# Kernel tuning notes

Hardware: AMD Instinct MI355X
Metric: run time of the kernel (lower is better)

The kernel has to match this reference:

```python
import jax, jax.numpy as jnp
import numpy as np

NUM_STEPS = 8
THRESHOLD = 0.5


def _glorot(key, shape):
    fan_in = shape[0]
    return jax.random.normal(key, shape, dtype=jnp.float32) / np.sqrt(fan_in).astype(np.float32)


def setup_inputs() -> dict:
    key = jax.random.key(0)
    ks = jax.random.split(key, 24)
    B, APM = 2048, 32           # molecules, atoms per molecule
    N = B * APM                 # 65536 nodes
    E = N * 4                   # 262144 directed edges
    NF, EF, NH, EH, MA = 64, 16, 128, 128, 256
    inp = {}
    inp['mol_a_reprs'] = jax.random.normal(ks[0], (B, MA), dtype=jnp.float32)
    inp['node_features'] = jax.random.normal(ks[1], (N, NF), dtype=jnp.float32)
    inp['edge_features'] = jax.random.normal(ks[2], (E, EF), dtype=jnp.float32)
    inp['node_hidden0'] = jnp.zeros((N, NH), dtype=jnp.float32)
    inp['edge_hidden0'] = jnp.zeros((E, EH), dtype=jnp.float32)
    inp['edges'] = jax.random.randint(ks[3], (2, E), 0, N, dtype=jnp.int32)
    inp['batch_indices'] = jnp.repeat(jnp.arange(B, dtype=jnp.int32), APM)  # sorted, in-range
    # MPN weights (no bias)
    inp['W1'] = _glorot(ks[4], (NF, EH))   # src node features -> edge hidden
    inp['W2'] = _glorot(ks[5], (EF, EH))   # edge features -> edge hidden
    inp['W3'] = _glorot(ks[6], (NH, EH))   # src node hidden -> edge hidden
    inp['U1'] = _glorot(ks[7], (NF, NH))   # node features -> node hidden
    inp['U2'] = _glorot(ks[8], (EH, NH))   # aggregated edge hidden -> node hidden
    # pick-atom MLP: (MA+NH)->256->128->64->1
    inp['M1w'] = _glorot(ks[9], (MA + NH, 256)); inp['M1b'] = jnp.zeros((256,), jnp.float32)
    inp['M2w'] = _glorot(ks[10], (256, 128));    inp['M2b'] = jnp.zeros((128,), jnp.float32)
    inp['M3w'] = _glorot(ks[11], (128, 64));     inp['M3b'] = jnp.zeros((64,), jnp.float32)
    inp['M4w'] = _glorot(ks[12], (64, 1));       inp['M4b'] = jnp.zeros((1,), jnp.float32)
    return inp


def _mpn(node_features, edge_features, node_h, edge_h, src, dst, W1, W2, W3, U1, U2):
    N = node_features.shape[0]
    W1x_src = node_features[src] @ W1          # [E, EH], loop-invariant
    W2e = edge_features @ W2                   # [E, EH], loop-invariant
    U1x = node_features @ U1                   # [N, NH], loop-invariant
    for _ in range(NUM_STEPS):
        agg = jax.ops.segment_sum(edge_h, dst, num_segments=N)   # [N, EH]
        node_h = jax.nn.relu(U1x + agg @ U2)                     # [N, NH]
        edge_h = jax.nn.relu(W1x_src + W2e + node_h[src] @ W3)   # [E, EH]
    return node_h


def reference(mol_a_reprs, node_features, edge_features, node_hidden0, edge_hidden0,
              edges, batch_indices, W1, W2, W3, U1, U2,
              M1w, M1b, M2w, M2b, M3w, M3b, M4w, M4b):
    src, dst = edges[0], edges[1]
    node_h = _mpn(node_features, edge_features, node_hidden0, edge_hidden0,
                  src, dst, W1, W2, W3, U1, U2)
    b_atom_mol_a = mol_a_reprs[batch_indices]                    # index_select gather [N, MA]
    x = jnp.concatenate([node_h, b_atom_mol_a], axis=1)          # [N, NH+MA]
    x = jax.nn.relu(x @ M1w + M1b)
    x = jax.nn.relu(x @ M2w + M2b)
    x = jax.nn.relu(x @ M3w + M3b)
    p = jax.nn.sigmoid(x @ M4w + M4b)                            # [N, 1]
    return p >= THRESHOLD
```

## Files before the change

kernel.cpp:

```cpp
#include <hip/hip_runtime.h>
#include <cstddef>

#define NF 64
#define EF 16
#define NH 128
#define EH 128
#define MA 256

static inline int ceil_div(int a, int b) { return (a + b - 1) / b; }

__global__ __launch_bounds__(256) void gemm_kernel(
    const float* __restrict__ A, const float* __restrict__ Bw,
    float* __restrict__ C,
    const float* __restrict__ addR, const int* __restrict__ addIdx,
    const float* __restrict__ bias,
    int M, int K, int Nc, int doRelu)
{
    __shared__ float As[16][64];
    __shared__ float Bs[16][64];
    const int tid = threadIdx.x;
    const int tx = tid & 15, ty = tid >> 4;
    const int m0 = blockIdx.y << 6;
    const int n0 = blockIdx.x << 6;
    const int lr = tid >> 2;
    const int lc = (tid & 3) << 2;
    const int bkr = tid >> 4;
    const int bc = (tid & 15) << 2;

    float acc[4][4];
#pragma unroll
    for (int i = 0; i < 4; ++i)
#pragma unroll
        for (int j = 0; j < 4; ++j) acc[i][j] = 0.0f;

    for (int k0 = 0; k0 < K; k0 += 16) {
        float4 a4 = *(const float4*)(A + (size_t)(m0 + lr) * K + (k0 + lc));
        float4 b4 = *(const float4*)(Bw + (size_t)(k0 + bkr) * Nc + (n0 + bc));
        __syncthreads();
        As[lc + 0][lr] = a4.x;
        As[lc + 1][lr] = a4.y;
        As[lc + 2][lr] = a4.z;
        As[lc + 3][lr] = a4.w;
        *(float4*)&Bs[bkr][bc] = b4;
        __syncthreads();
#pragma unroll
        for (int kk = 0; kk < 16; ++kk) {
            float a0 = As[kk][ty * 4 + 0];
            float a1 = As[kk][ty * 4 + 1];
            float a2 = As[kk][ty * 4 + 2];
            float a3 = As[kk][ty * 4 + 3];
            float b0 = Bs[kk][tx * 4 + 0];
            float b1 = Bs[kk][tx * 4 + 1];
            float b2 = Bs[kk][tx * 4 + 2];
            float b3 = Bs[kk][tx * 4 + 3];
            acc[0][0] += a0 * b0; acc[0][1] += a0 * b1; acc[0][2] += a0 * b2; acc[0][3] += a0 * b3;
            acc[1][0] += a1 * b0; acc[1][1] += a1 * b1; acc[1][2] += a1 * b2; acc[1][3] += a1 * b3;
            acc[2][0] += a2 * b0; acc[2][1] += a2 * b1; acc[2][2] += a2 * b2; acc[2][3] += a2 * b3;
            acc[3][0] += a3 * b0; acc[3][1] += a3 * b1; acc[3][2] += a3 * b2; acc[3][3] += a3 * b3;
        }
    }

    const int c = n0 + tx * 4;
    float4 bv = make_float4(0.f, 0.f, 0.f, 0.f);
    if (bias) bv = *(const float4*)(bias + c);
#pragma unroll
    for (int i = 0; i < 4; ++i) {
        int r = m0 + ty * 4 + i;
        float4 v = make_float4(acc[i][0], acc[i][1], acc[i][2], acc[i][3]);
        if (addR) {
            int ar = addIdx ? addIdx[r] : r;
            float4 ad = *(const float4*)(addR + (size_t)ar * Nc + c);
            v.x += ad.x; v.y += ad.y; v.z += ad.z; v.w += ad.w;
        }
        v.x += bv.x; v.y += bv.y; v.z += bv.z; v.w += bv.w;
        if (doRelu) {
            v.x = fmaxf(v.x, 0.f); v.y = fmaxf(v.y, 0.f);
            v.z = fmaxf(v.z, 0.f); v.w = fmaxf(v.w, 0.f);
        }
        *(float4*)(C + (size_t)r * Nc + c) = v;
    }
}

__global__ __launch_bounds__(256) void hist_kernel(const int* __restrict__ dst, int* __restrict__ deg, int E) {
    int e = blockIdx.x * 256 + threadIdx.x;
    if (e < E) atomicAdd(&deg[dst[e]], 1);
}

__global__ __launch_bounds__(256) void scan_block_kernel(const int* __restrict__ deg, int* __restrict__ rp,
                                                         int* __restrict__ bsum) {
    __shared__ int buf[256];
    int tid = threadIdx.x;
    int i = blockIdx.x * 256 + tid;
    int v = deg[i];
    buf[tid] = v;
    __syncthreads();
    for (int off = 1; off < 256; off <<= 1) {
        int t = (tid >= off) ? buf[tid - off] : 0;
        __syncthreads();
        buf[tid] += t;
        __syncthreads();
    }
    rp[i] = buf[tid] - v;
    if (tid == 255) bsum[blockIdx.x] = buf[255];
}

__global__ __launch_bounds__(256) void scan_top_kernel(const int* __restrict__ bsum, int* __restrict__ boff,
                                                       int* __restrict__ rp, int N) {
    __shared__ int buf[256];
    int tid = threadIdx.x;
    int v = bsum[tid];
    buf[tid] = v;
    __syncthreads();
    for (int off = 1; off < 256; off <<= 1) {
        int t = (tid >= off) ? buf[tid - off] : 0;
        __syncthreads();
        buf[tid] += t;
        __syncthreads();
    }
    boff[tid] = buf[tid] - v;
    if (tid == 255) rp[N] = buf[255];
}

__global__ __launch_bounds__(256) void scan_add_kernel(int* __restrict__ rp, int* __restrict__ cursor,
                                                       const int* __restrict__ boff) {
    int tid = threadIdx.x;
    int i = blockIdx.x * 256 + tid;
    int v = rp[i] + boff[blockIdx.x];
    rp[i] = v;
    cursor[i] = v;
}

__global__ __launch_bounds__(256) void scatter_kernel(const int* __restrict__ dst, int* __restrict__ cursor,
                                                      int* __restrict__ eid, int E) {
    int e = blockIdx.x * 256 + threadIdx.x;
    if (e < E) {
        int p = atomicAdd(&cursor[dst[e]], 1);
        eid[p] = e;
    }
}

__global__ __launch_bounds__(256) void relu_copy_kernel(const float* __restrict__ in, float* __restrict__ out, int n4) {
    int i = blockIdx.x * 256 + threadIdx.x;
    if (i < n4) {
        float4 v = ((const float4*)in)[i];
        v.x = fmaxf(v.x, 0.f); v.y = fmaxf(v.y, 0.f);
        v.z = fmaxf(v.z, 0.f); v.w = fmaxf(v.w, 0.f);
        ((float4*)out)[i] = v;
    }
}

__global__ __launch_bounds__(128) void agg_kernel(const float* __restrict__ nodeT, const float* __restrict__ W2e,
                                                  const int* __restrict__ rp, const int* __restrict__ eid,
                                                  const int* __restrict__ src, float* __restrict__ agg) {
    int n = blockIdx.x * 4 + threadIdx.y;
    int c = threadIdx.x << 2;
    int p0 = rp[n], p1 = rp[n + 1];
    float4 s = make_float4(0.f, 0.f, 0.f, 0.f);
    for (int p = p0; p < p1; ++p) {
        int e = eid[p];
        int sn = src[e];
        float4 t = *(const float4*)(nodeT + (size_t)sn * EH + c);
        float4 w = *(const float4*)(W2e + (size_t)e * EH + c);
        s.x += fmaxf(t.x + w.x, 0.f);
        s.y += fmaxf(t.y + w.y, 0.f);
        s.z += fmaxf(t.z + w.z, 0.f);
        s.w += fmaxf(t.w + w.w, 0.f);
    }
    *(float4*)(agg + (size_t)n * EH + c) = s;
}

__global__ __launch_bounds__(256) void final_kernel(const float* __restrict__ x3, const float* __restrict__ w,
                                                    const float* __restrict__ b, int* __restrict__ out, int Nn) {
    int g = blockIdx.x * 256 + threadIdx.x;
    int n = g >> 6;
    int lane = threadIdx.x & 63;
    if (n < Nn) {
        float v = x3[(size_t)n * 64 + lane] * w[lane];
#pragma unroll
        for (int off = 32; off > 0; off >>= 1) v += __shfl_xor(v, off, 64);
        if (lane == 0) out[n] = (v + b[0]) >= 0.f ? 1 : 0;
    }
}

extern "C" void kernel_launch(void* const* d_in, const int* in_sizes, int n_in,
                              void* d_out, int out_size, void* d_ws, size_t ws_size,
                              hipStream_t stream)
{
    const float* mol_a = (const float*)d_in[0];
    const float* nf    = (const float*)d_in[1];
    const float* ef    = (const float*)d_in[2];
    const int*   edges = (const int*)d_in[5];
    const int*   batch = (const int*)d_in[6];
    const float* W1  = (const float*)d_in[7];
    const float* W2  = (const float*)d_in[8];
    const float* W3  = (const float*)d_in[9];
    const float* U1  = (const float*)d_in[10];
    const float* U2  = (const float*)d_in[11];
    const float* M1w = (const float*)d_in[12];
    const float* M1b = (const float*)d_in[13];
    const float* M2w = (const float*)d_in[14];
    const float* M2b = (const float*)d_in[15];
    const float* M3w = (const float*)d_in[16];
    const float* M3b = (const float*)d_in[17];
    const float* M4w = (const float*)d_in[18];
    const float* M4b = (const float*)d_in[19];

    const int N = in_sizes[3] / NH;
    const int E = in_sizes[4] / EH;
    const int B = in_sizes[0] / MA;
    const int* srcp = edges;
    const int* dstp = edges + E;

    char* ws = (char*)d_ws;
    size_t off = 0;
    auto alloc = [&](size_t bytes) -> char* {
        char* p = ws + off;
        off = (off + bytes + 255) & ~(size_t)255;
        return p;
    };
    int* deg     = (int*)alloc((size_t)N * 4);
    int* rp      = (int*)alloc(((size_t)N + 1) * 4);
    int* cursor  = (int*)alloc((size_t)N * 4);
    int* bsum    = (int*)alloc(256 * 4);
    int* boff    = (int*)alloc(256 * 4);
    int* eid     = (int*)alloc((size_t)E * 4);
    float* nodePre = (float*)alloc((size_t)N * EH * 4);
    float* U1x     = (float*)alloc((size_t)N * NH * 4);
    float* node_h  = (float*)alloc((size_t)N * NH * 4);
    float* nodeT   = (float*)alloc((size_t)N * EH * 4);
    float* aggp    = (float*)alloc((size_t)N * EH * 4);
    float* molPart = (float*)alloc((size_t)B * 256 * 4);
    float* W2e     = (float*)alloc((size_t)E * EH * 4);
    float* x1 = (float*)W2e;
    float* x2 = nodeT;
    float* x3 = aggp;

    hipMemsetAsync(deg, 0, (size_t)N * 4, stream);
    hist_kernel<<<ceil_div(E, 256), 256, 0, stream>>>(dstp, deg, E);
    scan_block_kernel<<<N / 256, 256, 0, stream>>>(deg, rp, bsum);
    scan_top_kernel<<<1, 256, 0, stream>>>(bsum, boff, rp, N);
    scan_add_kernel<<<N / 256, 256, 0, stream>>>(rp, cursor, boff);
    scatter_kernel<<<ceil_div(E, 256), 256, 0, stream>>>(dstp, cursor, eid, E);

    gemm_kernel<<<dim3(EH / 64, N / 64), 256, 0, stream>>>(nf, W1, nodePre, nullptr, nullptr, nullptr, N, NF, EH, 0);
    gemm_kernel<<<dim3(EH / 64, E / 64), 256, 0, stream>>>(ef, W2, W2e, nullptr, nullptr, nullptr, E, EF, EH, 0);
    gemm_kernel<<<dim3(NH / 64, N / 64), 256, 0, stream>>>(nf, U1, U1x, nullptr, nullptr, nullptr, N, NF, NH, 0);

    relu_copy_kernel<<<(N * NH / 4) / 256, 256, 0, stream>>>(U1x, node_h, N * NH / 4);

    for (int s = 0; s < 7; ++s) {
        gemm_kernel<<<dim3(EH / 64, N / 64), 256, 0, stream>>>(node_h, W3, nodeT, nodePre, nullptr, nullptr, N, NH, EH, 0);
        agg_kernel<<<N / 4, dim3(32, 4), 0, stream>>>(nodeT, W2e, rp, eid, srcp, aggp);
        gemm_kernel<<<dim3(NH / 64, N / 64), 256, 0, stream>>>(aggp, U2, node_h, U1x, nullptr, nullptr, N, EH, NH, 1);
    }

    gemm_kernel<<<dim3(256 / 64, B / 64), 256, 0, stream>>>(mol_a, M1w + 128 * 256, molPart, nullptr, nullptr, M1b, B, MA, 256, 0);
    gemm_kernel<<<dim3(256 / 64, N / 64), 256, 0, stream>>>(node_h, M1w, x1, molPart, batch, nullptr, N, NH, 256, 1);
    gemm_kernel<<<dim3(128 / 64, N / 64), 256, 0, stream>>>(x1, M2w, x2, nullptr, nullptr, M2b, N, 256, 128, 1);
    gemm_kernel<<<dim3(64 / 64, N / 64), 256, 0, stream>>>(x2, M3w, x3, nullptr, nullptr, M3b, N, 128, 64, 1);
    final_kernel<<<ceil_div(N * 64, 256), 256, 0, stream>>>(x3, M4w, M4b, (int*)d_out, N);
}
```

Baseline: 1.445 ms.

## Add 128x128 GEMM tile kernel and pre-sort edge features by destination

Adds a 128x128-tile GEMM kernel in which each thread computes an 8x8 register block, and uses it for most GEMMs. This raises arithmetic intensity per shared-memory load compared with the 64x64 tile. The W2e projection is now computed with rows gathered in CSR (dst-sorted) order, and sorted source indices are stored during scatter. The aggregation loop can then stream W2e contiguously and skip the eid indirection. Larger tiles reduce the number of blocks (512 for the N-sized GEMMs) and raise register pressure, which could lower occupancy.

Result: faster. 1.387 ms (-4.0%).

```diff
diff --git a/kernel.cpp b/kernel.cpp
--- a/kernel.cpp
+++ b/kernel.cpp
@@ -8,6 +8,88 @@
 #define MA 256
 
 static inline int ceil_div(int a, int b) { return (a + b - 1) / b; }
+
+__global__ __launch_bounds__(256) void gemm128_kernel(
+    const float* __restrict__ A, const float* __restrict__ Bw,
+    float* __restrict__ C,
+    const float* __restrict__ addR, const int* __restrict__ addIdx,
+    const float* __restrict__ bias, const int* __restrict__ gatherA,
+    int M, int K, int Nc, int doRelu)
+{
+    __shared__ float As[16][132];
+    __shared__ float Bs[16][132];
+    const int tid = threadIdx.x;
+    const int tx = tid & 15;
+    const int ty = tid >> 4;
+    const int m0 = blockIdx.y << 7;
+    const int n0 = blockIdx.x << 7;
+
+    const int lr = tid >> 1;
+    const int lc = (tid & 1) << 3;
+    const int br = tid >> 4;
+    const int bc = (tid & 15) << 3;
+
+    float acc[8][8];
+#pragma unroll
+    for (int i = 0; i < 8; ++i)
+#pragma unroll
+        for (int j = 0; j < 8; ++j) acc[i][j] = 0.0f;
+
+    int arow = gatherA ? gatherA[m0 + lr] : (m0 + lr);
+    const float* aptr = A + (size_t)arow * K + lc;
+
+    for (int k0 = 0; k0 < K; k0 += 16) {
+        float4 a0 = *(const float4*)(aptr + k0);
+        float4 a1 = *(const float4*)(aptr + k0 + 4);
+        float4 b0 = *(const float4*)(Bw + (size_t)(k0 + br) * Nc + n0 + bc);
+        float4 b1 = *(const float4*)(Bw + (size_t)(k0 + br) * Nc + n0 + bc + 4);
+        __syncthreads();
+        As[lc + 0][lr] = a0.x; As[lc + 1][lr] = a0.y; As[lc + 2][lr] = a0.z; As[lc + 3][lr] = a0.w;
+        As[lc + 4][lr] = a1.x; As[lc + 5][lr] = a1.y; As[lc + 6][lr] = a1.z; As[lc + 7][lr] = a1.w;
+        *(float4*)&Bs[br][bc] = b0;
+        *(float4*)&Bs[br][bc + 4] = b1;
+        __syncthreads();
+#pragma unroll
+        for (int kk = 0; kk < 16; ++kk) {
+            float4 av0 = *(const float4*)&As[kk][ty * 8];
+            float4 av1 = *(const float4*)&As[kk][ty * 8 + 4];
+            float4 bv0 = *(const float4*)&Bs[kk][tx * 8];
+            float4 bv1 = *(const float4*)&Bs[kk][tx * 8 + 4];
+            float a[8] = {av0.x, av0.y, av0.z, av0.w, av1.x, av1.y, av1.z, av1.w};
+            float b[8] = {bv0.x, bv0.y, bv0.z, bv0.w, bv1.x, bv1.y, bv1.z, bv1.w};
+#pragma unroll
+            for (int i = 0; i < 8; ++i)
+#pragma unroll
+                for (int j = 0; j < 8; ++j)
+                    acc[i][j] = fmaf(a[i], b[j], acc[i][j]);
+        }
+    }
+
+    const int c = n0 + tx * 8;
+    float4 bvl = make_float4(0.f, 0.f, 0.f, 0.f), bvh = bvl;
+    if (bias) { bvl = *(const float4*)(bias + c); bvh = *(const float4*)(bias + c + 4); }
+#pragma unroll
+    for (int i = 0; i < 8; ++i) {
+        int r = m0 + ty * 8 + i;
+        float4 vl = make_float4(acc[i][0], acc[i][1], acc[i][2], acc[i][3]);
+        float4 vh = make_float4(acc[i][4], acc[i][5], acc[i][6], acc[i][7]);
+        if (addR) {
+            int ar = addIdx ? addIdx[r] : r;
+            float4 al = *(const float4*)(addR + (size_t)ar * Nc + c);
+            float4 ah = *(const float4*)(addR + (size_t)ar * Nc + c + 4);
+            vl.x += al.x; vl.y += al.y; vl.z += al.z; vl.w += al.w;
+            vh.x += ah.x; vh.y += ah.y; vh.z += ah.z; vh.w += ah.w;
+        }
+        vl.x += bvl.x; vl.y += bvl.y; vl.z += bvl.z; vl.w += bvl.w;
+        vh.x += bvh.x; vh.y += bvh.y; vh.z += bvh.z; vh.w += bvh.w;
+        if (doRelu) {
+            vl.x = fmaxf(vl.x, 0.f); vl.y = fmaxf(vl.y, 0.f); vl.z = fmaxf(vl.z, 0.f); vl.w = fmaxf(vl.w, 0.f);
+            vh.x = fmaxf(vh.x, 0.f); vh.y = fmaxf(vh.y, 0.f); vh.z = fmaxf(vh.z, 0.f); vh.w = fmaxf(vh.w, 0.f);
+        }
+        *(float4*)(C + (size_t)r * Nc + c) = vl;
+        *(float4*)(C + (size_t)r * Nc + c + 4) = vh;
+    }
+}
 
 __global__ __launch_bounds__(256) void gemm_kernel(
     const float* __restrict__ A, const float* __restrict__ Bw,
@@ -130,12 +212,14 @@
     cursor[i] = v;
 }
 
-__global__ __launch_bounds__(256) void scatter_kernel(const int* __restrict__ dst, int* __restrict__ cursor,
-                                                      int* __restrict__ eid, int E) {
+__global__ __launch_bounds__(256) void scatter_kernel(const int* __restrict__ dst, const int* __restrict__ src,
+                                                      int* __restrict__ cursor,
+                                                      int* __restrict__ eid, int* __restrict__ srcS, int E) {
     int e = blockIdx.x * 256 + threadIdx.x;
     if (e < E) {
         int p = atomicAdd(&cursor[dst[e]], 1);
         eid[p] = e;
+        srcS[p] = src[e];
     }
 }
 
@@ -149,18 +233,17 @@
     }
 }
 
-__global__ __launch_bounds__(128) void agg_kernel(const float* __restrict__ nodeT, const float* __restrict__ W2e,
-                                                  const int* __restrict__ rp, const int* __restrict__ eid,
-                                                  const int* __restrict__ src, float* __restrict__ agg) {
+__global__ __launch_bounds__(128) void agg_kernel(const float* __restrict__ nodeT, const float* __restrict__ W2eS,
+                                                  const int* __restrict__ rp, const int* __restrict__ srcS,
+                                                  float* __restrict__ agg) {
     int n = blockIdx.x * 4 + threadIdx.y;
     int c = threadIdx.x << 2;
     int p0 = rp[n], p1 = rp[n + 1];
     float4 s = make_float4(0.f, 0.f, 0.f, 0.f);
     for (int p = p0; p < p1; ++p) {
-        int e = eid[p];
-        int sn = src[e];
+        int sn = srcS[p];
         float4 t = *(const float4*)(nodeT + (size_t)sn * EH + c);
-        float4 w = *(const float4*)(W2e + (size_t)e * EH + c);
+        float4 w = *(const float4*)(W2eS + (size_t)p * EH + c);
         s.x += fmaxf(t.x + w.x, 0.f);
         s.y += fmaxf(t.y + w.y, 0.f);
         s.z += fmaxf(t.z + w.z, 0.f);
@@ -224,14 +307,15 @@
     int* bsum    = (int*)alloc(256 * 4);
     int* boff    = (int*)alloc(256 * 4);
     int* eid     = (int*)alloc((size_t)E * 4);
+    int* srcS    = (int*)alloc((size_t)E * 4);
     float* nodePre = (float*)alloc((size_t)N * EH * 4);
     float* U1x     = (float*)alloc((size_t)N * NH * 4);
     float* node_h  = (float*)alloc((size_t)N * NH * 4);
     float* nodeT   = (float*)alloc((size_t)N * EH * 4);
     float* aggp    = (float*)alloc((size_t)N * EH * 4);
     float* molPart = (float*)alloc((size_t)B * 256 * 4);
-    float* W2e     = (float*)alloc((size_t)E * EH * 4);
-    float* x1 = (float*)W2e;
+    float* W2eS    = (float*)alloc((size_t)E * EH * 4);
+    float* x1 = (float*)W2eS;
     float* x2 = nodeT;
     float* x3 = aggp;
 
@@ -240,23 +324,23 @@
     scan_block_kernel<<<N / 256, 256, 0, stream>>>(deg, rp, bsum);
     scan_top_kernel<<<1, 256, 0, stream>>>(bsum, boff, rp, N);
     scan_add_kernel<<<N / 256, 256, 0, stream>>>(rp, cursor, boff);
-    scatter_kernel<<<ceil_div(E, 256), 256, 0, stream>>>(dstp, cursor, eid, E);
-
-    gemm_kernel<<<dim3(EH / 64, N / 64), 256, 0, stream>>>(nf, W1, nodePre, nullptr, nullptr, nullptr, N, NF, EH, 0);
-    gemm_kernel<<<dim3(EH / 64, E / 64), 256, 0, stream>>>(ef, W2, W2e, nullptr, nullptr, nullptr, E, EF, EH, 0);
-    gemm_kernel<<<dim3(NH / 64, N / 64), 256, 0, stream>>>(nf, U1, U1x, nullptr, nullptr, nullptr, N, NF, NH, 0);
+    scatter_kernel<<<ceil_div(E, 256), 256, 0, stream>>>(dstp, srcp, cursor, eid, srcS, E);
+
+    gemm128_kernel<<<dim3(1, N / 128), 256, 0, stream>>>(nf, W1, nodePre, nullptr, nullptr, nullptr, nullptr, N, NF, EH, 0);
+    gemm128_kernel<<<dim3(1, E / 128), 256, 0, stream>>>(ef, W2, W2eS, nullptr, nullptr, nullptr, eid, E, EF, EH, 0);
+    gemm128_kernel<<<dim3(1, N / 128), 256, 0, stream>>>(nf, U1, U1x, nullptr, nullptr, nullptr, nullptr, N, NF, NH, 0);
 
     relu_copy_kernel<<<(N * NH / 4) / 256, 256, 0, stream>>>(U1x, node_h, N * NH / 4);
 
     for (int s = 0; s < 7; ++s) {
-        gemm_kernel<<<dim3(EH / 64, N / 64), 256, 0, stream>>>(node_h, W3, nodeT, nodePre, nullptr, nullptr, N, NH, EH, 0);
-        agg_kernel<<<N / 4, dim3(32, 4), 0, stream>>>(nodeT, W2e, rp, eid, srcp, aggp);
-        gemm_kernel<<<dim3(NH / 64, N / 64), 256, 0, stream>>>(aggp, U2, node_h, U1x, nullptr, nullptr, N, EH, NH, 1);
+        gemm128_kernel<<<dim3(1, N / 128), 256, 0, stream>>>(node_h, W3, nodeT, nodePre, nullptr, nullptr, nullptr, N, NH, EH, 0);
+        agg_kernel<<<N / 4, dim3(32, 4), 0, stream>>>(nodeT, W2eS, rp, srcS, aggp);
+        gemm128_kernel<<<dim3(1, N / 128), 256, 0, stream>>>(aggp, U2, node_h, U1x, nullptr, nullptr, nullptr, N, EH, NH, 1);
     }
 
     gemm_kernel<<<dim3(256 / 64, B / 64), 256, 0, stream>>>(mol_a, M1w + 128 * 256, molPart, nullptr, nullptr, M1b, B, MA, 256, 0);
-    gemm_kernel<<<dim3(256 / 64, N / 64), 256, 0, stream>>>(node_h, M1w, x1, molPart, batch, nullptr, N, NH, 256, 1);
-    gemm_kernel<<<dim3(128 / 64, N / 64), 256, 0, stream>>>(x1, M2w, x2, nullptr, nullptr, M2b, N, 256, 128, 1);
-    gemm_kernel<<<dim3(64 / 64, N / 64), 256, 0, stream>>>(x2, M3w, x3, nullptr, nullptr, M3b, N, 128, 64, 1);
+    gemm128_kernel<<<dim3(2, N / 128), 256, 0, stream>>>(node_h, M1w, x1, molPart, batch, nullptr, nullptr, N, NH, 256, 1);
+    gemm128_kernel<<<dim3(1, N / 128), 256, 0, stream>>>(x1, M2w, x2, nullptr, nullptr, M2b, nullptr, N, 256, 128, 1);
+    gemm_kernel<<<dim3(1, N / 64), 256, 0, stream>>>(x2, M3w, x3, nullptr, nullptr, M3b, N, 128, 64, 1);
     final_kernel<<<ceil_div(N * 64, 256), 256, 0, stream>>>(x3, M4w, M4b, (int*)d_out, N);
 }
```
